# Kernel tuning notes

Hardware: AMD Instinct MI355X
Metric: run time of the kernel (lower is better)

## Reference

```python
import jax, jax.numpy as jnp
import numpy as np

C_IN, C_HID, N_HEADS = 128, 32, 4
INF = 1.0e9
LN_EPS = 1e-5


def setup_inputs() -> dict:
    key = jax.random.key(0)
    ks = jax.random.split(key, 12)
    B, I, J, C, H, D = 1, 384, 384, C_IN, N_HEADS, C_HID
    s = 0.02
    return {
        "x": jax.random.normal(ks[0], (B, I, J, C), dtype=jnp.float32),
        "mask": jnp.ones((B, I, J), dtype=jnp.float32),
        "ln_g": jnp.ones((C,), dtype=jnp.float32),
        "ln_b": jnp.zeros((C,), dtype=jnp.float32),
        "w_tri": jax.random.normal(ks[1], (C, H), dtype=jnp.float32) * s,
        "wq": jax.random.normal(ks[2], (C, H, D), dtype=jnp.float32) * s,
        "wk": jax.random.normal(ks[3], (C, H, D), dtype=jnp.float32) * s,
        "wv": jax.random.normal(ks[4], (C, H, D), dtype=jnp.float32) * s,
        "wg": jax.random.normal(ks[5], (C, H, D), dtype=jnp.float32) * s,
        "bg": jnp.ones((H, D), dtype=jnp.float32),
        "wo": jax.random.normal(ks[6], (H, D, C), dtype=jnp.float32) * s,
        "bo": jnp.zeros((C,), dtype=jnp.float32),
    }


def reference(x, mask, ln_g, ln_b, w_tri, wq, wk, wv, wg, bg, wo, bo):
    # LayerNorm over channel dim
    mu = jnp.mean(x, axis=-1, keepdims=True)
    var = jnp.mean(jnp.square(x - mu), axis=-1, keepdims=True)
    xn = (x - mu) * jax.lax.rsqrt(var + LN_EPS) * ln_g + ln_b  # [B,I,J,C]

    # mask bias: [B, I, 1, 1, J]
    mask_bias = (INF * (mask - 1.0))[..., :, None, None, :]
    # triangle bias: linear(x) -> [B,I,J,H] -> [B,1,H,I,J]
    tri_bias = jnp.einsum("bijc,ch->bhij", xn, w_tri)[:, None]

    scale = 1.0 / jnp.sqrt(jnp.asarray(C_HID, dtype=xn.dtype))
    # per-row attention over J: tensors [B, I, H, J, D]
    q = jnp.einsum("bixc,chd->bihxd", xn, wq) * scale
    k = jnp.einsum("bixc,chd->bihxd", xn, wk)
    v = jnp.einsum("bixc,chd->bihxd", xn, wv)

    logits = jnp.einsum("bihqd,bihkd->bihqk", q, k) + mask_bias + tri_bias
    a = jax.nn.softmax(logits, axis=-1)
    o = jnp.einsum("bihqk,bihkd->bihqd", a, v)  # [B,I,H,J,D]

    g = jax.nn.sigmoid(jnp.einsum("bixc,chd->bihxd", xn, wg) + bg[None, None, :, None, :])
    o = o * g
    out = jnp.einsum("bihxd,hdc->bixc", o, wo) + bo  # [B,I,J,C]
    return out
```

## Files before the change

### kernel.cpp

```cpp
#include <hip/hip_runtime.h>
#include <math.h>


#define I_DIM 384
#define J_DIM 384
#define C_DIM 128
#define H_DIM 4
#define D_DIM 32
#define NPOS (I_DIM * J_DIM)
#define Q_SCALE 0.17677669529663687f

typedef __attribute__((ext_vector_type(8))) short bf16x8;
typedef __attribute__((ext_vector_type(4))) float f32x4;

__device__ __forceinline__ float sigmoidf_(float v) {
    return 1.0f / (1.0f + __expf(-v));
}
__device__ __forceinline__ unsigned short f2bf(float f) {
    union { float f; unsigned u; } x; x.f = f;
    unsigned u = x.u;
    u += 0x7fffu + ((u >> 16) & 1u);
    return (unsigned short)(u >> 16);
}
__device__ __forceinline__ float bf2f(unsigned short v) {
    union { unsigned u; float f; } x; x.u = ((unsigned)v) << 16;
    return x.f;
}

__global__ __launch_bounds__(256) void prep_kernel(
    const float* __restrict__ wq, const float* __restrict__ wk,
    const float* __restrict__ wv, const float* __restrict__ wg,
    const float* __restrict__ wo, unsigned short* __restrict__ Wt)
{
    const int mat = blockIdx.x;
    const float* W = (mat == 0) ? wq : (mat == 1) ? wk : (mat == 2) ? wv
                    : (mat == 3) ? wg : wo;
    const float scale = (mat == 0) ? Q_SCALE : 1.0f;
    const int t = threadIdx.x;
    const int n = t >> 1, c0 = (t & 1) * 64;
#pragma unroll
    for (int u = 0; u < 8; ++u) {
        unsigned pk[4];
#pragma unroll
        for (int w = 0; w < 4; ++w) {
            const unsigned short a = f2bf(W[(size_t)(c0 + u * 8 + w * 2 + 0) * 128 + n] * scale);
            const unsigned short b = f2bf(W[(size_t)(c0 + u * 8 + w * 2 + 1) * 128 + n] * scale);
            pk[w] = (unsigned)a | ((unsigned)b << 16);
        }
        int4 q; q.x = pk[0]; q.y = pk[1]; q.z = pk[2]; q.w = pk[3];
        *(int4*)(Wt + (size_t)mat * 16384 + n * 128 + c0 + u * 8) = q;
    }
}

__global__ __launch_bounds__(256) void ln_kernel(
    const float* __restrict__ x, const float* __restrict__ ln_g,
    const float* __restrict__ ln_b, const float* __restrict__ w_tri,
    unsigned short* __restrict__ xn, float* __restrict__ tri)
{
    const int t = threadIdx.x;
    const int g = t >> 2, q = t & 3;
    const int pos = blockIdx.x * 64 + g;
    const float* xrow = x + (size_t)pos * C_DIM + q * 32;

    float xv[32];
    float s = 0.f, ss = 0.f;
#pragma unroll
    for (int u = 0; u < 8; ++u) {
        float4 v4 = ((const float4*)xrow)[u];
        xv[u * 4 + 0] = v4.x; xv[u * 4 + 1] = v4.y;
        xv[u * 4 + 2] = v4.z; xv[u * 4 + 3] = v4.w;
        s  += v4.x + v4.y + v4.z + v4.w;
        ss += v4.x * v4.x + v4.y * v4.y + v4.z * v4.z + v4.w * v4.w;
    }
    s  += __shfl_xor(s, 1);  s  += __shfl_xor(s, 2);
    ss += __shfl_xor(ss, 1); ss += __shfl_xor(ss, 2);
    const float mu  = s * (1.0f / 128.0f);
    const float var = ss * (1.0f / 128.0f) - mu * mu;
    const float rstd = rsqrtf(var + 1e-5f);

    float ptri[4] = {0.f, 0.f, 0.f, 0.f};
    unsigned short* xdst = xn + (size_t)pos * C_DIM + q * 32;
#pragma unroll
    for (int u2 = 0; u2 < 4; ++u2) {
        const int cb = q * 32 + u2 * 8;
        const float4 g0 = *(const float4*)(ln_g + cb);
        const float4 g1 = *(const float4*)(ln_g + cb + 4);
        const float4 b0 = *(const float4*)(ln_b + cb);
        const float4 b1 = *(const float4*)(ln_b + cb + 4);
        float xn8[8];
        xn8[0] = (xv[u2 * 8 + 0] - mu) * rstd * g0.x + b0.x;
        xn8[1] = (xv[u2 * 8 + 1] - mu) * rstd * g0.y + b0.y;
        xn8[2] = (xv[u2 * 8 + 2] - mu) * rstd * g0.z + b0.z;
        xn8[3] = (xv[u2 * 8 + 3] - mu) * rstd * g0.w + b0.w;
        xn8[4] = (xv[u2 * 8 + 4] - mu) * rstd * g1.x + b1.x;
        xn8[5] = (xv[u2 * 8 + 5] - mu) * rstd * g1.y + b1.y;
        xn8[6] = (xv[u2 * 8 + 6] - mu) * rstd * g1.z + b1.z;
        xn8[7] = (xv[u2 * 8 + 7] - mu) * rstd * g1.w + b1.w;
#pragma unroll
        for (int w = 0; w < 8; ++w) {
            const float4 wt = ((const float4*)w_tri)[cb + w];
            ptri[0] += xn8[w] * wt.x; ptri[1] += xn8[w] * wt.y;
            ptri[2] += xn8[w] * wt.z; ptri[3] += xn8[w] * wt.w;
        }
        unsigned pk[4];
#pragma unroll
        for (int w = 0; w < 4; ++w)
            pk[w] = (unsigned)f2bf(xn8[w * 2]) | ((unsigned)f2bf(xn8[w * 2 + 1]) << 16);
        int4 q4; q4.x = pk[0]; q4.y = pk[1]; q4.z = pk[2]; q4.w = pk[3];
        *(int4*)(xdst + u2 * 8) = q4;
    }
#pragma unroll
    for (int hh = 0; hh < 4; ++hh) {
        ptri[hh] += __shfl_xor(ptri[hh], 1);
        ptri[hh] += __shfl_xor(ptri[hh], 2);
    }
    const int i = pos / J_DIM, j = pos - (pos / J_DIM) * J_DIM;
    tri[((size_t)q * I_DIM + i) * J_DIM + j] = ptri[q];
}

__global__ __launch_bounds__(256) void tri_tr_kernel(float* __restrict__ tri)
{
    const int h = blockIdx.x / 78;
    int rem = blockIdx.x - h * 78;
    int ti = 0;
    while (rem >= 12 - ti) { rem -= 12 - ti; ++ti; }
    const int tj = ti + rem;

    float* T = tri + (size_t)h * I_DIM * J_DIM;
    __shared__ float A[32][33];
    __shared__ float B[32][33];

    const int t = threadIdx.x;
    const int r = t >> 3, c4 = (t & 7) * 4;

    {
        const float4 v = *(const float4*)(T + (size_t)(ti * 32 + r) * J_DIM + tj * 32 + c4);
        A[r][c4 + 0] = v.x; A[r][c4 + 1] = v.y; A[r][c4 + 2] = v.z; A[r][c4 + 3] = v.w;
        const float4 w = *(const float4*)(T + (size_t)(tj * 32 + r) * J_DIM + ti * 32 + c4);
        B[r][c4 + 0] = w.x; B[r][c4 + 1] = w.y; B[r][c4 + 2] = w.z; B[r][c4 + 3] = w.w;
    }
    __syncthreads();
    {
        float4 v;
        v.x = B[c4 + 0][r]; v.y = B[c4 + 1][r]; v.z = B[c4 + 2][r]; v.w = B[c4 + 3][r];
        *(float4*)(T + (size_t)(ti * 32 + r) * J_DIM + tj * 32 + c4) = v;
        float4 w;
        w.x = A[c4 + 0][r]; w.y = A[c4 + 1][r]; w.z = A[c4 + 2][r]; w.w = A[c4 + 3][r];
        *(float4*)(T + (size_t)(tj * 32 + r) * J_DIM + ti * 32 + c4) = w;
    }
}

__global__ __launch_bounds__(256) void pgemm_kernel(
    const unsigned short* __restrict__ xn, const unsigned short* __restrict__ Wt,
    const float* __restrict__ bg,
    unsigned short* __restrict__ qb, unsigned short* __restrict__ kb,
    unsigned short* __restrict__ vb, unsigned short* __restrict__ gb)
{
    __shared__ unsigned short At[128 * 128];
    __shared__ unsigned short Bt[128 * 128];

    const int t = threadIdx.x;
    const int pos0 = blockIdx.x * 128;
    const int lane = t & 63, wave = t >> 6;
    const int q15 = lane & 15, quad = lane >> 4;

    {
        const int r = t >> 1, half = t & 1;
        const unsigned short* src = xn + (size_t)(pos0 + r) * C_DIM + half * 64;
#pragma unroll
        for (int u = 0; u < 8; ++u) {
            const int c = half * 8 + u;
            *(int4*)&At[r * 128 + ((c ^ (r & 7)) * 8)] = *(const int4*)(src + u * 8);
        }
    }

    const int m0 = wave * 32;
    for (int mat = 0; mat < 4; ++mat) {
        __syncthreads();
        {
            const int rn = t >> 1, half = t & 1;
            const unsigned short* src = Wt + (size_t)mat * 16384 + rn * 128 + half * 64;
#pragma unroll
            for (int u = 0; u < 8; ++u) {
                const int c = half * 8 + u;
                *(int4*)&Bt[rn * 128 + ((c ^ (rn & 7)) * 8)] = *(const int4*)(src + u * 8);
            }
        }
        __syncthreads();

        f32x4 acc[2][8];
#pragma unroll
        for (int mt = 0; mt < 2; ++mt)
#pragma unroll
            for (int nt = 0; nt < 8; ++nt) acc[mt][nt] = (f32x4){0.f, 0.f, 0.f, 0.f};

#pragma unroll
        for (int kk = 0; kk < 4; ++kk) {
            const int sw = ((kk * 4 + quad) ^ (q15 & 7)) * 8;
            const bf16x8 a0 = *(const bf16x8*)&At[(m0 + q15) * 128 + sw];
            const bf16x8 a1 = *(const bf16x8*)&At[(m0 + 16 + q15) * 128 + sw];
#pragma unroll
            for (int nt = 0; nt < 8; ++nt) {
                const bf16x8 b = *(const bf16x8*)&Bt[(nt * 16 + q15) * 128 + sw];
                acc[0][nt] = __builtin_amdgcn_mfma_f32_16x16x32_bf16(a0, b, acc[0][nt], 0, 0, 0);
                acc[1][nt] = __builtin_amdgcn_mfma_f32_16x16x32_bf16(a1, b, acc[1][nt], 0, 0, 0);
            }
        }

        __syncthreads();
#pragma unroll
        for (int mt = 0; mt < 2; ++mt)
#pragma unroll
            for (int nt = 0; nt < 8; ++nt) {
                const int col = nt * 16 + q15;
                const float bgl = (mat == 3) ? bg[col] : 0.f;
#pragma unroll
                for (int reg = 0; reg < 4; ++reg) {
                    float v = acc[mt][nt][reg];
                    if (mat == 3) v = sigmoidf_(v + bgl);
                    const int row = m0 + mt * 16 + quad * 4 + reg;
                    Bt[row * 128 + (((col >> 3) ^ (row & 7)) * 8) + (col & 7)] = f2bf(v);
                }
            }
        __syncthreads();
        {
            unsigned short* O = (mat == 0) ? qb : (mat == 1) ? kb : (mat == 2) ? vb : gb;
#pragma unroll
            for (int sgm = 0; sgm < 2; ++sgm) {
                const int ch = t + sgm * 256;
                const int r = ch >> 2, hh = ch & 3;
                const int pos = pos0 + r;
                const int i = pos / J_DIM, j = pos - (pos / J_DIM) * J_DIM;
                unsigned short* dst = O + (((size_t)i * H_DIM + hh) * J_DIM + j) * D_DIM;
#pragma unroll
                for (int w = 0; w < 4; ++w) {
                    const int c = hh * 4 + w;
                    *(int4*)(dst + w * 8) = *(const int4*)&Bt[r * 128 + ((c ^ (r & 7)) * 8)];
                }
            }
        }
    }
}

__global__ __launch_bounds__(256) void attn_kernel(
    const unsigned short* __restrict__ qb, const unsigned short* __restrict__ kb,
    const unsigned short* __restrict__ vb, unsigned short* gob,
    const float* __restrict__ triT, const float* __restrict__ mask)
{
    __shared__ unsigned short Klds[64 * 32];
    __shared__ unsigned short Vt[32 * 68];
    __shared__ unsigned short Plds[4][32 * 68];
    __shared__ float Mb[J_DIM];

    const int t = threadIdx.x;
    const int lane = t & 63, wave = t >> 6;
    const int q15 = lane & 15, quad = lane >> 4;
    const int i = blockIdx.x >> 2, h = blockIdx.x & 3;
    const size_t hb = (size_t)(i * H_DIM + h) * (J_DIM * D_DIM);
    const int m0 = wave * 96;

    for (int idx = t; idx < J_DIM; idx += 256)
        Mb[idx] = 1.0e9f * (mask[i * J_DIM + idx] - 1.0f);

    bf16x8 qf[6];
#pragma unroll
    for (int m = 0; m < 6; ++m)
        qf[m] = *(const bf16x8*)(qb + hb + (size_t)(m0 + m * 16 + q15) * D_DIM + quad * 8);

    f32x4 Oacc[6][2];
    float sums[6][4];
#pragma unroll
    for (int m = 0; m < 6; ++m) {
#pragma unroll
        for (int d2 = 0; d2 < 2; ++d2) Oacc[m][d2] = (f32x4){0.f, 0.f, 0.f, 0.f};
#pragma unroll
        for (int r = 0; r < 4; ++r) sums[m][r] = 0.f;
    }

    unsigned short* Pw = Plds[wave];
    const float* triH = triT + (size_t)h * J_DIM * I_DIM;

    for (int kt = 0; kt < 6; ++kt) {
        __syncthreads();
        {
            const int kp = t >> 2, du = (t & 3) * 8;
            const size_t gsrc = hb + (size_t)(kt * 64 + kp) * D_DIM + du;
            *(int4*)&Klds[kp * 32 + du] = *(const int4*)(kb + gsrc);
            int4 vv = *(const int4*)(vb + gsrc);
            const unsigned short* vs = (const unsigned short*)&vv;
#pragma unroll
            for (int u = 0; u < 8; ++u)
                Vt[(du + u) * 68 + kp] = vs[u];
        }
        __syncthreads();

        bf16x8 vf[2][2];
#pragma unroll
        for (int ks = 0; ks < 2; ++ks)
#pragma unroll
            for (int d2 = 0; d2 < 2; ++d2)
                vf[ks][d2] = *(const bf16x8*)&Vt[(d2 * 16 + q15) * 68 + ks * 32 + quad * 8];

#pragma unroll
        for (int pass = 0; pass < 3; ++pass) {
            const int mbase = pass * 2;

#pragma unroll
            for (int nt = 0; nt < 4; ++nt) {
                const bf16x8 kf = *(const bf16x8*)&Klds[(nt * 16 + q15) * 32 + quad * 8];
                const float mb = Mb[kt * 64 + nt * 16 + q15];
                const float* tcol = triH + (size_t)(kt * 64 + nt * 16 + q15) * I_DIM;
#pragma unroll
                for (int mm = 0; mm < 2; ++mm) {
                    const int m = mbase + mm;
                    const float4 tb = *(const float4*)(tcol + m0 + m * 16 + quad * 4);
                    f32x4 s = {0.f, 0.f, 0.f, 0.f};
                    s = __builtin_amdgcn_mfma_f32_16x16x32_bf16(qf[m], kf, s, 0, 0, 0);
                    const float p0 = __expf(s[0] + mb + tb.x);
                    const float p1 = __expf(s[1] + mb + tb.y);
                    const float p2 = __expf(s[2] + mb + tb.z);
                    const float p3 = __expf(s[3] + mb + tb.w);
                    sums[m][0] += p0; sums[m][1] += p1;
                    sums[m][2] += p2; sums[m][3] += p3;
                    const int row = mm * 16 + quad * 4;
                    const int col = nt * 16 + q15;
                    Pw[(row + 0) * 68 + col] = f2bf(p0);
                    Pw[(row + 1) * 68 + col] = f2bf(p1);
                    Pw[(row + 2) * 68 + col] = f2bf(p2);
                    Pw[(row + 3) * 68 + col] = f2bf(p3);
                }
            }

#pragma unroll
            for (int mm = 0; mm < 2; ++mm) {
                const int m = mbase + mm;
#pragma unroll
                for (int ks = 0; ks < 2; ++ks) {
                    const bf16x8 af = *(const bf16x8*)&Pw[(mm * 16 + q15) * 68 + ks * 32 + quad * 8];
                    Oacc[m][0] = __builtin_amdgcn_mfma_f32_16x16x32_bf16(af, vf[ks][0], Oacc[m][0], 0, 0, 0);
                    Oacc[m][1] = __builtin_amdgcn_mfma_f32_16x16x32_bf16(af, vf[ks][1], Oacc[m][1], 0, 0, 0);
                }
            }
        }
    }

    float inv[6][4];
#pragma unroll
    for (int m = 0; m < 6; ++m)
#pragma unroll
        for (int r = 0; r < 4; ++r) {
            float s0 = sums[m][r];
            s0 += __shfl_xor(s0, 1); s0 += __shfl_xor(s0, 2);
            s0 += __shfl_xor(s0, 4); s0 += __shfl_xor(s0, 8);
            inv[m][r] = 1.0f / s0;
        }

#pragma unroll
    for (int m = 0; m < 6; ++m) {
        const int qrow = m0 + m * 16 + quad * 4;
#pragma unroll
        for (int d2 = 0; d2 < 2; ++d2) {
            const int d = d2 * 16 + q15;
#pragma unroll
            for (int r = 0; r < 4; ++r) {
                const size_t idx = hb + (size_t)(qrow + r) * D_DIM + d;
                const float g = bf2f(gob[idx]);
                gob[idx] = f2bf(Oacc[m][d2][r] * inv[m][r] * g);
            }
        }
    }
}

__global__ __launch_bounds__(256) void out_kernel(
    const unsigned short* __restrict__ og, const unsigned short* __restrict__ WtO,
    const float* __restrict__ bo, float* __restrict__ out)
{
    __shared__ unsigned short At[128 * 128];
    __shared__ unsigned short Bt[128 * 128];

    const int t = threadIdx.x;
    const int pos0 = blockIdx.x * 128;
    const int lane = t & 63, wave = t >> 6;
    const int q15 = lane & 15, quad = lane >> 4;

    {
        const int r = t >> 1, half = t & 1;
        const int pos = pos0 + r;
        const int i = pos / J_DIM, j = pos - (pos / J_DIM) * J_DIM;
#pragma unroll
        for (int u = 0; u < 8; ++u) {
            const int k0 = half * 64 + u * 8;
            const int hh = k0 >> 5, d0 = k0 & 31;
            const int4 v = *(const int4*)(og + (((size_t)i * H_DIM + hh) * J_DIM + j) * D_DIM + d0);
            const int c = half * 8 + u;
            *(int4*)&At[r * 128 + ((c ^ (r & 7)) * 8)] = v;
        }
        const unsigned short* src = WtO + r * 128 + half * 64;
#pragma unroll
        for (int u = 0; u < 8; ++u) {
            const int c = half * 8 + u;
            *(int4*)&Bt[r * 128 + ((c ^ (r & 7)) * 8)] = *(const int4*)(src + u * 8);
        }
    }
    __syncthreads();

    const int m0 = wave * 32;
    f32x4 acc[2][8];
#pragma unroll
    for (int mt = 0; mt < 2; ++mt)
#pragma unroll
        for (int nt = 0; nt < 8; ++nt) acc[mt][nt] = (f32x4){0.f, 0.f, 0.f, 0.f};

#pragma unroll
    for (int kk = 0; kk < 4; ++kk) {
        const int sw = ((kk * 4 + quad) ^ (q15 & 7)) * 8;
        const bf16x8 a0 = *(const bf16x8*)&At[(m0 + q15) * 128 + sw];
        const bf16x8 a1 = *(const bf16x8*)&At[(m0 + 16 + q15) * 128 + sw];
#pragma unroll
        for (int nt = 0; nt < 8; ++nt) {
            const bf16x8 b = *(const bf16x8*)&Bt[(nt * 16 + q15) * 128 + sw];
            acc[0][nt] = __builtin_amdgcn_mfma_f32_16x16x32_bf16(a0, b, acc[0][nt], 0, 0, 0);
            acc[1][nt] = __builtin_amdgcn_mfma_f32_16x16x32_bf16(a1, b, acc[1][nt], 0, 0, 0);
        }
    }

#pragma unroll
    for (int mt = 0; mt < 2; ++mt)
#pragma unroll
        for (int nt = 0; nt < 8; ++nt) {
            const float bov = bo[nt * 16 + q15];
#pragma unroll
            for (int reg = 0; reg < 4; ++reg) {
                const int pos = pos0 + m0 + mt * 16 + quad * 4 + reg;
                out[(size_t)pos * C_DIM + nt * 16 + q15] = acc[mt][nt][reg] + bov;
            }
        }
}

extern "C" void kernel_launch(void* const* d_in, const int* in_sizes, int n_in,
                              void* d_out, int out_size, void* d_ws, size_t ws_size,
                              hipStream_t stream)
{
    const float* x     = (const float*)d_in[0];
    const float* mask  = (const float*)d_in[1];
    const float* ln_g  = (const float*)d_in[2];
    const float* ln_b  = (const float*)d_in[3];
    const float* w_tri = (const float*)d_in[4];
    const float* wq    = (const float*)d_in[5];
    const float* wk    = (const float*)d_in[6];
    const float* wv    = (const float*)d_in[7];
    const float* wg    = (const float*)d_in[8];
    const float* bg    = (const float*)d_in[9];
    const float* wo    = (const float*)d_in[10];
    const float* bo    = (const float*)d_in[11];
    float* out = (float*)d_out;
    char* ws = (char*)d_ws;

    const size_t NE = (size_t)NPOS * 128;
    unsigned short* qb = (unsigned short*)ws;
    unsigned short* kb = (unsigned short*)(ws + NE * 2);
    unsigned short* vb = (unsigned short*)(ws + NE * 4);
    unsigned short* gb = (unsigned short*)(ws + NE * 6);
    float*         tri = (float*)(ws + NE * 8);
    unsigned short* Wt = (unsigned short*)(ws + NE * 8 + (size_t)NPOS * 4 * 4);
    unsigned short* xn = Wt + 5 * 16384;

    prep_kernel<<<5, 256, 0, stream>>>(wq, wk, wv, wg, wo, Wt);
    ln_kernel<<<NPOS / 64, 256, 0, stream>>>(x, ln_g, ln_b, w_tri, xn, tri);
    tri_tr_kernel<<<H_DIM * 78, 256, 0, stream>>>(tri);
    pgemm_kernel<<<NPOS / 128, 256, 0, stream>>>(xn, Wt, bg, qb, kb, vb, gb);
    attn_kernel<<<I_DIM * H_DIM, 256, 0, stream>>>(qb, kb, vb, gb, tri, mask);
    out_kernel<<<NPOS / 128, 256, 0, stream>>>(gb, Wt + 4 * 16384, bo, out);
}
```

Measured before the change: 476.7 us.

## Assign one head per wave in attention kernel to drop block barriers

```diff
diff --git a/kernel.cpp b/kernel.cpp
--- a/kernel.cpp
+++ b/kernel.cpp
@@ -247,25 +247,27 @@
     const unsigned short* __restrict__ vb, unsigned short* gob,
     const float* __restrict__ triT, const float* __restrict__ mask)
 {
-    __shared__ unsigned short Klds[64 * 32];
-    __shared__ unsigned short Vt[32 * 68];
+    __shared__ unsigned short Klds[4][64 * 32];
+    __shared__ unsigned short Vt[4][32 * 68];
     __shared__ unsigned short Plds[4][32 * 68];
     __shared__ float Mb[J_DIM];
 
     const int t = threadIdx.x;
     const int lane = t & 63, wave = t >> 6;
     const int q15 = lane & 15, quad = lane >> 4;
-    const int i = blockIdx.x >> 2, h = blockIdx.x & 3;
+    const int i = blockIdx.x >> 2, qq = blockIdx.x & 3;
+    const int q0 = qq * 96;
+    const int h = wave;
     const size_t hb = (size_t)(i * H_DIM + h) * (J_DIM * D_DIM);
-    const int m0 = wave * 96;
 
     for (int idx = t; idx < J_DIM; idx += 256)
         Mb[idx] = 1.0e9f * (mask[i * J_DIM + idx] - 1.0f);
+    __syncthreads();
 
     bf16x8 qf[6];
 #pragma unroll
     for (int m = 0; m < 6; ++m)
-        qf[m] = *(const bf16x8*)(qb + hb + (size_t)(m0 + m * 16 + q15) * D_DIM + quad * 8);
+        qf[m] = *(const bf16x8*)(qb + hb + (size_t)(q0 + m * 16 + q15) * D_DIM + quad * 8);
 
     f32x4 Oacc[6][2];
     float sums[6][4];
@@ -277,29 +279,42 @@
         for (int r = 0; r < 4; ++r) sums[m][r] = 0.f;
     }
 
+    unsigned short* Kw = Klds[wave];
+    unsigned short* Vw = Vt[wave];
     unsigned short* Pw = Plds[wave];
     const float* triH = triT + (size_t)h * J_DIM * I_DIM;
 
     for (int kt = 0; kt < 6; ++kt) {
-        __syncthreads();
         {
-            const int kp = t >> 2, du = (t & 3) * 8;
-            const size_t gsrc = hb + (size_t)(kt * 64 + kp) * D_DIM + du;
-            *(int4*)&Klds[kp * 32 + du] = *(const int4*)(kb + gsrc);
-            int4 vv = *(const int4*)(vb + gsrc);
-            const unsigned short* vs = (const unsigned short*)&vv;
-#pragma unroll
-            for (int u = 0; u < 8; ++u)
-                Vt[(du + u) * 68 + kp] = vs[u];
-        }
-        __syncthreads();
+            const size_t gsrc = hb + (size_t)(kt * 64 + lane) * D_DIM;
+            const int4 k0 = *(const int4*)(kb + gsrc);
+            const int4 k1 = *(const int4*)(kb + gsrc + 8);
+            const int4 k2 = *(const int4*)(kb + gsrc + 16);
+            const int4 k3 = *(const int4*)(kb + gsrc + 24);
+            *(int4*)&Kw[lane * 32 + 0]  = k0;
+            *(int4*)&Kw[lane * 32 + 8]  = k1;
+            *(int4*)&Kw[lane * 32 + 16] = k2;
+            *(int4*)&Kw[lane * 32 + 24] = k3;
+            int4 vv[4];
+            vv[0] = *(const int4*)(vb + gsrc);
+            vv[1] = *(const int4*)(vb + gsrc + 8);
+            vv[2] = *(const int4*)(vb + gsrc + 16);
+            vv[3] = *(const int4*)(vb + gsrc + 24);
+#pragma unroll
+            for (int p = 0; p < 4; ++p) {
+                const unsigned short* vs = (const unsigned short*)&vv[p];
+#pragma unroll
+                for (int u = 0; u < 8; ++u)
+                    Vw[(p * 8 + u) * 68 + lane] = vs[u];
+            }
+        }
 
         bf16x8 vf[2][2];
 #pragma unroll
         for (int ks = 0; ks < 2; ++ks)
 #pragma unroll
             for (int d2 = 0; d2 < 2; ++d2)
-                vf[ks][d2] = *(const bf16x8*)&Vt[(d2 * 16 + q15) * 68 + ks * 32 + quad * 8];
+                vf[ks][d2] = *(const bf16x8*)&Vw[(d2 * 16 + q15) * 68 + ks * 32 + quad * 8];
 
 #pragma unroll
         for (int pass = 0; pass < 3; ++pass) {
@@ -307,13 +322,13 @@
 
 #pragma unroll
             for (int nt = 0; nt < 4; ++nt) {
-                const bf16x8 kf = *(const bf16x8*)&Klds[(nt * 16 + q15) * 32 + quad * 8];
+                const bf16x8 kf = *(const bf16x8*)&Kw[(nt * 16 + q15) * 32 + quad * 8];
                 const float mb = Mb[kt * 64 + nt * 16 + q15];
                 const float* tcol = triH + (size_t)(kt * 64 + nt * 16 + q15) * I_DIM;
 #pragma unroll
                 for (int mm = 0; mm < 2; ++mm) {
                     const int m = mbase + mm;
-                    const float4 tb = *(const float4*)(tcol + m0 + m * 16 + quad * 4);
+                    const float4 tb = *(const float4*)(tcol + q0 + m * 16 + quad * 4);
                     f32x4 s = {0.f, 0.f, 0.f, 0.f};
                     s = __builtin_amdgcn_mfma_f32_16x16x32_bf16(qf[m], kf, s, 0, 0, 0);
                     const float p0 = __expf(s[0] + mb + tb.x);
@@ -357,7 +372,7 @@
 
 #pragma unroll
     for (int m = 0; m < 6; ++m) {
-        const int qrow = m0 + m * 16 + quad * 4;
+        const int qrow = q0 + m * 16 + quad * 4;
 #pragma unroll
         for (int d2 = 0; d2 < 2; ++d2) {
             const int d = d2 * 16 + q15;
```

Result: no change. 481.5 us (+1.0%).

## Read projection weights directly from global and store outputs without LDS staging

Applied to the files above, without the earlier changes.

```diff
diff --git a/kernel.cpp b/kernel.cpp
--- a/kernel.cpp
+++ b/kernel.cpp
@@ -157,7 +157,6 @@
     unsigned short* __restrict__ vb, unsigned short* __restrict__ gb)
 {
     __shared__ unsigned short At[128 * 128];
-    __shared__ unsigned short Bt[128 * 128];
 
     const int t = threadIdx.x;
     const int pos0 = blockIdx.x * 128;
@@ -173,20 +172,11 @@
             *(int4*)&At[r * 128 + ((c ^ (r & 7)) * 8)] = *(const int4*)(src + u * 8);
         }
     }
+    __syncthreads();
 
     const int m0 = wave * 32;
     for (int mat = 0; mat < 4; ++mat) {
-        __syncthreads();
-        {
-            const int rn = t >> 1, half = t & 1;
-            const unsigned short* src = Wt + (size_t)mat * 16384 + rn * 128 + half * 64;
-#pragma unroll
-            for (int u = 0; u < 8; ++u) {
-                const int c = half * 8 + u;
-                *(int4*)&Bt[rn * 128 + ((c ^ (rn & 7)) * 8)] = *(const int4*)(src + u * 8);
-            }
-        }
-        __syncthreads();
+        const unsigned short* WtM = Wt + (size_t)mat * 16384;
 
         f32x4 acc[2][8];
 #pragma unroll
@@ -199,46 +189,30 @@
             const int sw = ((kk * 4 + quad) ^ (q15 & 7)) * 8;
             const bf16x8 a0 = *(const bf16x8*)&At[(m0 + q15) * 128 + sw];
             const bf16x8 a1 = *(const bf16x8*)&At[(m0 + 16 + q15) * 128 + sw];
+            const unsigned short* bp = WtM + q15 * 128 + (kk * 4 + quad) * 8;
 #pragma unroll
             for (int nt = 0; nt < 8; ++nt) {
-                const bf16x8 b = *(const bf16x8*)&Bt[(nt * 16 + q15) * 128 + sw];
+                const bf16x8 b = *(const bf16x8*)(bp + nt * 16 * 128);
                 acc[0][nt] = __builtin_amdgcn_mfma_f32_16x16x32_bf16(a0, b, acc[0][nt], 0, 0, 0);
                 acc[1][nt] = __builtin_amdgcn_mfma_f32_16x16x32_bf16(a1, b, acc[1][nt], 0, 0, 0);
             }
         }
 
-        __syncthreads();
+        unsigned short* O = (mat == 0) ? qb : (mat == 1) ? kb : (mat == 2) ? vb : gb;
 #pragma unroll
         for (int mt = 0; mt < 2; ++mt)
 #pragma unroll
-            for (int nt = 0; nt < 8; ++nt) {
-                const int col = nt * 16 + q15;
-                const float bgl = (mat == 3) ? bg[col] : 0.f;
-#pragma unroll
-                for (int reg = 0; reg < 4; ++reg) {
+            for (int reg = 0; reg < 4; ++reg) {
+                const int pos = pos0 + m0 + mt * 16 + quad * 4 + reg;
+                const int i = pos / J_DIM, j = pos - (pos / J_DIM) * J_DIM;
+                unsigned short* rowp = O + ((size_t)i * H_DIM * J_DIM + j) * D_DIM;
+#pragma unroll
+                for (int nt = 0; nt < 8; ++nt) {
                     float v = acc[mt][nt][reg];
-                    if (mat == 3) v = sigmoidf_(v + bgl);
-                    const int row = m0 + mt * 16 + quad * 4 + reg;
-                    Bt[row * 128 + (((col >> 3) ^ (row & 7)) * 8) + (col & 7)] = f2bf(v);
+                    if (mat == 3) v = sigmoidf_(v + bg[nt * 16 + q15]);
+                    rowp[(nt >> 1) * (J_DIM * D_DIM) + (nt & 1) * 16 + q15] = f2bf(v);
                 }
             }
-        __syncthreads();
-        {
-            unsigned short* O = (mat == 0) ? qb : (mat == 1) ? kb : (mat == 2) ? vb : gb;
-#pragma unroll
-            for (int sgm = 0; sgm < 2; ++sgm) {
-                const int ch = t + sgm * 256;
-                const int r = ch >> 2, hh = ch & 3;
-                const int pos = pos0 + r;
-                const int i = pos / J_DIM, j = pos - (pos / J_DIM) * J_DIM;
-                unsigned short* dst = O + (((size_t)i * H_DIM + hh) * J_DIM + j) * D_DIM;
-#pragma unroll
-                for (int w = 0; w < 4; ++w) {
-                    const int c = hh * 4 + w;
-                    *(int4*)(dst + w * 8) = *(const int4*)&Bt[r * 128 + ((c ^ (r & 7)) * 8)];
-                }
-            }
-        }
     }
 }
 
```

New measurement: 528.7 us. +10.9%, slower.
